# Performance work log

Measured on AMD Instinct MI355X. Metric: run time of the kernel, lower is better.

Reference implementation:

```python
import jax, jax.numpy as jnp
import numpy as np

NUM_HEADS = 8
TOPK = 16


def setup_inputs() -> dict:
    key = jax.random.key(0)
    ks = jax.random.split(key, 13)
    B, C, H, W = 2, 512, 64, 64
    Hu, Wu = H // 2, W // 2
    hd = C // NUM_HEADS
    n = lambda k, shape, s=1.0: jax.random.normal(k, shape, dtype=jnp.float32) * s
    return {
        "x": n(ks[0], (B, C, H, W)),
        "upper_feat": n(ks[1], (B, C, Hu, Wu)),
        "gumbel": jax.random.gumbel(ks[2], (B, NUM_HEADS, Hu * Wu), dtype=jnp.float32),
        # 1x1 convs (Conv2d + folded eval-mode BN => weight matrix + bias)
        "q_w": n(ks[3], (C, C), 0.02), "q_b": n(ks[4], (C,), 0.02),
        "kv_w": n(ks[5], (2 * C, C), 0.02), "kv_b": n(ks[6], (2 * C,), 0.02),
        "proj_w": n(ks[7], (C, C), 0.02), "proj_b": n(ks[8], (C,), 0.02),
        # depthwise 7x7 PE conv (groups = C)
        "pe_w": n(ks[9], (C, 1, 7, 7), 0.02), "pe_b": n(ks[10], (C,), 0.02),
        # gate conv1d kernel_size=1: [head_dim, 2*head_dim]
        "gate_w": n(ks[11], (hd, 2 * hd), 0.02), "gate_b": n(ks[12], (hd,), 0.02),
    }


def reference(x, upper_feat, gumbel, q_w, q_b, kv_w, kv_b, proj_w, proj_b,
              pe_w, pe_b, gate_w, gate_b):
    B, C, H, W = x.shape
    hd = C // NUM_HEADS
    Hu, Wu = upper_feat.shape[2], upper_feat.shape[3]
    N, Nu = H * W, Hu * Wu
    scale = hd ** -0.5

    def conv1x1(t, w, b):
        return jnp.einsum('bchw,oc->bohw', t, w) + b[None, :, None, None]

    # coarse attention: q from x, k/v from upper_feat
    q = conv1x1(x, q_w, q_b).reshape(B, NUM_HEADS, hd, N).transpose(0, 1, 3, 2)          # [B,h,N,d]
    kv = conv1x1(upper_feat, kv_w, kv_b).reshape(B, NUM_HEADS, 2 * hd, Nu).transpose(0, 1, 3, 2)
    k, v = kv[..., :hd], kv[..., hd:]                                                    # [B,h,Nu,d]
    sim = jnp.einsum('bhnd,bhmd->bhnm', q, k) * scale                                    # [B,h,N,Nu]
    attn = jax.nn.softmax(sim, axis=-1)
    coarse = jnp.einsum('bhnm,bhmd->bhnd', attn, v)                                      # [B,h,N,d]

    # fine branch: kv from x, top-k token selection via gumbel-softmax scores
    f_kv = conv1x1(x, kv_w, kv_b).reshape(B, NUM_HEADS, 2 * hd, N).transpose(0, 1, 3, 2)
    f_k, f_v = f_kv[..., :hd], f_kv[..., hd:]                                            # [B,h,N,d]

    # heat: channel-mean of x, adaptive-avg-pooled 2x2 to upper resolution (no grad)
    heat = jax.lax.stop_gradient(
        x.mean(axis=1).reshape(B, Hu, 2, Wu, 2).mean(axis=(2, 4)).reshape(B, Nu))
    global_sim = sim.mean(axis=2) * heat[:, None, :]                                     # [B,h,Nu]
    soft_weights = jax.nn.softmax(global_sim + gumbel, axis=-1)
    _, idx = jax.lax.top_k(soft_weights, TOPK)                                           # [B,h,K]

    # map each selected upper-token to its 2x2 block of x-tokens
    h_idx = (idx // Wu) * 2
    w_idx = (idx % Wu) * 2
    idx_full = jnp.concatenate(
        [(h_idx + dh) * W + (w_idx + dw) for dh in range(2) for dw in range(2)], axis=-1)  # [B,h,4K]

    topk_k = jnp.take_along_axis(f_k, idx_full[..., None], axis=2)                       # [B,h,4K,d]
    topk_v = jnp.take_along_axis(f_v, idx_full[..., None], axis=2)
    fine = jax.nn.softmax(jnp.einsum('bhnd,bhmd->bhnm', q, topk_k) * scale, axis=-1)
    refined = jnp.einsum('bhnm,bhmd->bhnd', fine, topk_v)                                # [B,h,N,d]

    # gated fusion (conv1d kernel_size=1 == per-token linear over 2d channels)
    fusion = jnp.concatenate([coarse, refined], axis=-1)                                 # [B,h,N,2d]
    gate = jax.nn.sigmoid(jnp.einsum('bhnc,oc->bhno', fusion, gate_w) + gate_b)
    out = gate * refined + (1.0 - gate) * coarse                                         # [B,h,N,d]

    x_out = out.transpose(0, 1, 3, 2).reshape(B, C, H, W)

    # positional encoding: depthwise 7x7 conv on v, bilinear upsample to (H,W)
    v_rs = v.transpose(0, 1, 3, 2).reshape(B, C, Hu, Wu)
    v_pe = jax.lax.conv_general_dilated(
        v_rs, pe_w, (1, 1), ((3, 3), (3, 3)), feature_group_count=C,
        dimension_numbers=('NCHW', 'OIHW', 'NCHW')) + pe_b[None, :, None, None]
    v_pe = jax.image.resize(v_pe, (B, C, H, W), method='bilinear')

    return conv1x1(x_out + v_pe, proj_w, proj_b)
```

## Files before the change

### kernel.cpp

```cpp
#include <hip/hip_runtime.h>
#include <hip/hip_bf16.h>
#include <cstdint>

typedef __hip_bfloat16 bf16;
typedef unsigned short u16;
typedef __attribute__((ext_vector_type(8))) short bf16x8;
typedef __attribute__((ext_vector_type(4))) float f32x4;

static __device__ __forceinline__ float bs2f(u16 s) {
  unsigned int u = ((unsigned int)s) << 16;
  float f;
  __builtin_memcpy(&f, &u, 4);
  return f;
}
static __device__ __forceinline__ u16 f2bs(float f) {
  bf16 h = __float2bfloat16(f);
  u16 s;
  __builtin_memcpy(&s, &h, 2);
  return s;
}
static __device__ __forceinline__ float ldf(const void* p, size_t i, int f32) {
  return f32 ? ((const float*)p)[i] : bs2f(((const u16*)p)[i]);
}

__global__ __launch_bounds__(256) void detect_dtype(const uint4* __restrict__ xs,
                                                    int* __restrict__ flag) {
  int i = blockIdx.x * 256 + threadIdx.x;
  uint4 v = xs[i];
  bool hit = false;
#pragma unroll
  for (int j = 0; j < 4; ++j) {
    unsigned w = (j == 0) ? v.x : (j == 1) ? v.y : (j == 2) ? v.z : v.w;
    if ((w & 0x7F80u) == 0x7F80u) hit = true;
    if ((w & 0x7F800000u) == 0x7F800000u) hit = true;
  }
  unsigned long long mask = __ballot(hit);
  if (mask != 0ull && (threadIdx.x & 63) == 0) atomicOr(flag, 1);
}

__global__ __launch_bounds__(256) void prep_gate(
    const void* __restrict__ gate_w, const void* __restrict__ gate_b,
    u16* __restrict__ gwb, float* __restrict__ gbf,
    const int* __restrict__ dtf) {
  const int f32 = *dtf;
  int t = threadIdx.x;
  for (int i = t; i < 8192; i += 256)
    gwb[i] = f32 ? f2bs(((const float*)gate_w)[i]) : ((const u16*)gate_w)[i];
  if (t < 64) gbf[t] = ldf(gate_b, t, f32);
}

__global__ __launch_bounds__(256) void transpose_bf16(
    const void* __restrict__ src, u16* __restrict__ dst, int N,
    float* __restrict__ heat, const int* __restrict__ dtf) {
  const int f32 = *dtf;
  const int b = blockIdx.z, n0 = blockIdx.x * 64, c0 = blockIdx.y * 64;
  const int t = threadIdx.x;
  __shared__ __align__(16) u16 tile[64][72];
#pragma unroll
  for (int j = 0; j < 2; ++j) {
    int cc = (t >> 3) + j * 32;
    int nn = (t & 7) * 8;
    u16 tmp[8];
    if (f32) {
      const float* s4 = (const float*)src + ((size_t)(b * 512 + c0 + cc)) * N + n0 + nn;
#pragma unroll
      for (int u = 0; u < 8; ++u) tmp[u] = f2bs(s4[u]);
    } else {
      *reinterpret_cast<uint4*>(tmp) = *reinterpret_cast<const uint4*>(
          (const u16*)src + ((size_t)(b * 512 + c0 + cc)) * N + n0 + nn);
    }
    *reinterpret_cast<uint4*>(&tile[cc][nn]) = *reinterpret_cast<const uint4*>(tmp);
  }
  __syncthreads();
  if (heat != nullptr && t < 32) {
    float s = 0.f;
#pragma unroll 8
    for (int cc = 0; cc < 64; ++cc)
      s += bs2f(tile[cc][2 * t]) + bs2f(tile[cc][2 * t + 1]);
    int y = blockIdx.x;
    atomicAdd(&heat[b * 1024 + (y >> 1) * 32 + t], s);
  }
#pragma unroll
  for (int j = 0; j < 2; ++j) {
    int nn = (t >> 3) + j * 32;
    int cc0 = (t & 7) * 8;
    u16 tmp[8];
#pragma unroll
    for (int u = 0; u < 8; ++u) tmp[u] = tile[cc0 + u][nn];
    *reinterpret_cast<uint4*>(&dst[((size_t)b * N + n0 + nn) * 512 + c0 + cc0]) =
        *reinterpret_cast<const uint4*>(tmp);
  }
}

template<int MODE>
__global__ __launch_bounds__(256) void gemm128(
    const u16* __restrict__ A, const void* __restrict__ W,
    const void* __restrict__ bias, u16* __restrict__ o0,
    void* __restrict__ ob, float* __restrict__ qsum, int M,
    const int* __restrict__ dtf) {
  const int f32 = *dtf;
  const int b = blockIdx.z, m0 = blockIdx.x * 128, oo0 = blockIdx.y * 64;
  const int t = threadIdx.x, w = t >> 6, lane = t & 63;
  const int quad = lane >> 4, c = lane & 15;
  __shared__ __align__(16) u16 As[128][72];
  __shared__ __align__(16) u16 Ws[64][72];
  f32x4 acc[2][4];
#pragma unroll
  for (int nt = 0; nt < 2; ++nt)
#pragma unroll
    for (int ot = 0; ot < 4; ++ot) acc[nt][ot] = (f32x4){0.f, 0.f, 0.f, 0.f};
  const u16* Ab = A + (size_t)b * M * 512;
  const int arow = t >> 1, acol = (t & 1) * 32;
  const int wrow = t >> 2, wcol = (t & 3) * 16;

  for (int k0 = 0; k0 < 512; k0 += 64) {
    __syncthreads();
    {
      const u16* ga = Ab + (size_t)(m0 + arow) * 512 + k0 + acol;
      uint4* ad = reinterpret_cast<uint4*>(&As[arow][acol]);
      const uint4* gs = reinterpret_cast<const uint4*>(ga);
      ad[0] = gs[0]; ad[1] = gs[1]; ad[2] = gs[2]; ad[3] = gs[3];
      if (f32) {
        const float* gw = (const float*)W + (size_t)(oo0 + wrow) * 512 + k0 + wcol;
#pragma unroll
        for (int e = 0; e < 16; ++e) Ws[wrow][wcol + e] = f2bs(gw[e]);
      } else {
        const u16* gw = (const u16*)W + (size_t)(oo0 + wrow) * 512 + k0 + wcol;
        *reinterpret_cast<uint4*>(&Ws[wrow][wcol])     = *reinterpret_cast<const uint4*>(gw);
        *reinterpret_cast<uint4*>(&Ws[wrow][wcol + 8]) = *reinterpret_cast<const uint4*>(gw + 8);
      }
    }
    __syncthreads();
#pragma unroll
    for (int ks = 0; ks < 2; ++ks) {
      bf16x8 av[2];
      av[0] = *reinterpret_cast<const bf16x8*>(&As[w * 32 + c][ks * 32 + quad * 8]);
      av[1] = *reinterpret_cast<const bf16x8*>(&As[w * 32 + 16 + c][ks * 32 + quad * 8]);
#pragma unroll
      for (int ot = 0; ot < 4; ++ot) {
        bf16x8 wv = *reinterpret_cast<const bf16x8*>(&Ws[ot * 16 + c][ks * 32 + quad * 8]);
#pragma unroll
        for (int nt = 0; nt < 2; ++nt) {
          if (MODE == 3)
            acc[nt][ot] = __builtin_amdgcn_mfma_f32_16x16x32_bf16(wv, av[nt], acc[nt][ot], 0, 0, 0);
          else
            acc[nt][ot] = __builtin_amdgcn_mfma_f32_16x16x32_bf16(av[nt], wv, acc[nt][ot], 0, 0, 0);
        }
      }
    }
  }

  if (MODE == 0) {
    const int h = oo0 >> 6, bh = b * 8 + h;
#pragma unroll
    for (int ot = 0; ot < 4; ++ot) {
      int o = oo0 + ot * 16 + c;
      int d = o & 63;
      float bv = ldf(bias, o, f32);
      float qs = 0.f;
#pragma unroll
      for (int nt = 0; nt < 2; ++nt)
#pragma unroll
        for (int r = 0; r < 4; ++r) {
          int m = m0 + w * 32 + nt * 16 + quad * 4 + r;
          u16 val = f2bs(acc[nt][ot][r] + bv);
          o0[((size_t)bh * M + m) * 64 + d] = val;
          qs += bs2f(val);
        }
      qs += __shfl_xor(qs, 16, 64);
      qs += __shfl_xor(qs, 32, 64);
      if (quad == 0) atomicAdd(&qsum[bh * 64 + d], qs);
    }
  } else {
#pragma unroll
    for (int ot = 0; ot < 4; ++ot)
#pragma unroll
      for (int r = 0; r < 4; ++r) {
        int o = oo0 + ot * 16 + quad * 4 + r;
        float bv = ldf(bias, o, f32);
#pragma unroll
        for (int nt = 0; nt < 2; ++nt) {
          int m = m0 + w * 32 + nt * 16 + c;
          float val = acc[nt][ot][r] + bv;
          size_t oi_ = ((size_t)(b * 512 + o)) * M + m;
          if (f32) ((float*)ob)[oi_] = val;
          else     ((u16*)ob)[oi_] = f2bs(val);
        }
      }
  }
}

__global__ __launch_bounds__(256) void gemm_kv(
    const u16* __restrict__ A, const void* __restrict__ W,
    const void* __restrict__ bias, u16* __restrict__ kb, u16* __restrict__ vTb,
    int M, const int* __restrict__ dtf) {
  const int f32 = *dtf;
  const int b = blockIdx.z, m0 = blockIdx.x * 64, oo0 = blockIdx.y * 64;
  const int t = threadIdx.x, w = t >> 6, lane = t & 63;
  const int quad = lane >> 4, c = lane & 15;
  __shared__ __align__(16) u16 As[64][72];
  __shared__ __align__(16) u16 Ws[64][72];
  f32x4 acc[4];
#pragma unroll
  for (int ot = 0; ot < 4; ++ot) acc[ot] = (f32x4){0.f, 0.f, 0.f, 0.f};
  const u16* Ab = A + (size_t)b * M * 512;
  const int srow = t >> 2, scol = (t & 3) * 16;

  for (int k0 = 0; k0 < 512; k0 += 64) {
    __syncthreads();
    {
      const u16* ga = Ab + (size_t)(m0 + srow) * 512 + k0 + scol;
      *reinterpret_cast<uint4*>(&As[srow][scol])     = *reinterpret_cast<const uint4*>(ga);
      *reinterpret_cast<uint4*>(&As[srow][scol + 8]) = *reinterpret_cast<const uint4*>(ga + 8);
      if (f32) {
        const float* gw = (const float*)W + (size_t)(oo0 + srow) * 512 + k0 + scol;
#pragma unroll
        for (int e = 0; e < 16; ++e) Ws[srow][scol + e] = f2bs(gw[e]);
      } else {
        const u16* gw = (const u16*)W + (size_t)(oo0 + srow) * 512 + k0 + scol;
        *reinterpret_cast<uint4*>(&Ws[srow][scol])     = *reinterpret_cast<const uint4*>(gw);
        *reinterpret_cast<uint4*>(&Ws[srow][scol + 8]) = *reinterpret_cast<const uint4*>(gw + 8);
      }
    }
    __syncthreads();
#pragma unroll
    for (int ks = 0; ks < 2; ++ks) {
      bf16x8 av = *reinterpret_cast<const bf16x8*>(&As[w * 16 + c][ks * 32 + quad * 8]);
#pragma unroll
      for (int ot = 0; ot < 4; ++ot) {
        bf16x8 wv = *reinterpret_cast<const bf16x8*>(&Ws[ot * 16 + c][ks * 32 + quad * 8]);
        acc[ot] = __builtin_amdgcn_mfma_f32_16x16x32_bf16(av, wv, acc[ot], 0, 0, 0);
      }
    }
  }

#pragma unroll
  for (int ot = 0; ot < 4; ++ot) {
    int o = oo0 + ot * 16 + c;
    float bv = ldf(bias, o, f32);
    int hh = o >> 7, jj = o & 127;
#pragma unroll
    for (int r = 0; r < 4; ++r) {
      int m = m0 + w * 16 + quad * 4 + r;
      u16 val = f2bs(acc[ot][r] + bv);
      if (jj < 64) kb[((size_t)(b * 8 + hh) * M + m) * 64 + jj] = val;
      else         vTb[((size_t)(b * 8 + hh) * 64 + (jj & 63)) * M + m] = val;
    }
  }
}

__global__ __launch_bounds__(256) void topk_kernel(
    const float* __restrict__ qsum, const u16* __restrict__ k,
    const float* __restrict__ heat, const void* __restrict__ gumbel,
    int* __restrict__ posb, const int* __restrict__ dtf) {
  const int f32 = *dtf;
  int bh = blockIdx.x, b = bh >> 3, t = threadIdx.x;
  __shared__ float qs[64];
  __shared__ float s[1024];
  __shared__ float rv[256];
  __shared__ int   ri[256];
  if (t < 64) qs[t] = qsum[bh * 64 + t];
  __syncthreads();
  for (int j = 0; j < 4; ++j) {
    int m = t + j * 256;
    const u16* kr = k + ((size_t)bh * 1024 + m) * 64;
    float dot = 0.f;
    for (int d = 0; d < 64; ++d) dot += qs[d] * bs2f(kr[d]);
    s[m] = dot * (0.125f / 4096.0f) * (heat[b * 1024 + m] * (1.0f / 2048.0f)) +
           ldf(gumbel, (size_t)bh * 1024 + m, f32);
  }
  __syncthreads();
  for (int it = 0; it < 16; ++it) {
    float bv = -1e30f; int bi = 0x7fffffff;
    for (int j = 0; j < 4; ++j) {
      int m = t + j * 256; float vv = s[m];
      if (vv > bv || (vv == bv && m < bi)) { bv = vv; bi = m; }
    }
    rv[t] = bv; ri[t] = bi; __syncthreads();
    for (int off = 128; off; off >>= 1) {
      if (t < off) {
        if (rv[t + off] > rv[t] || (rv[t + off] == rv[t] && ri[t + off] < ri[t])) {
          rv[t] = rv[t + off]; ri[t] = ri[t + off];
        }
      }
      __syncthreads();
    }
    if (t == 0) {
      int mi = ri[0]; s[mi] = -1e30f;
      int hy = (mi >> 5) * 2, wx = (mi & 31) * 2;
      posb[bh * 64 + it]      = hy * 64 + wx;
      posb[bh * 64 + 16 + it] = hy * 64 + wx + 1;
      posb[bh * 64 + 32 + it] = (hy + 1) * 64 + wx;
      posb[bh * 64 + 48 + it] = (hy + 1) * 64 + wx + 1;
    }
    __syncthreads();
  }
}

__global__ __launch_bounds__(256) void gather_kv_mfma(
    const u16* __restrict__ xT, const void* __restrict__ kv_w,
    const void* __restrict__ kv_b, const int* __restrict__ posb,
    u16* __restrict__ tkb, u16* __restrict__ tvTb,
    const int* __restrict__ dtf) {
  const int f32 = *dtf;
  const int bh = blockIdx.x, b = bh >> 3, h = bh & 7;
  const int half = blockIdx.y;
  const int t = threadIdx.x, w = t >> 6, lane = t & 63;
  const int quad = lane >> 4, c = lane & 15;
  __shared__ int pos[64];
  __shared__ __align__(16) u16 As[64][72];
  __shared__ __align__(16) u16 Ws[64][72];
  if (t < 64) pos[t] = posb[bh * 64 + t];
  __syncthreads();
  const int obase = h * 128 + half * 64;
  const int srow = t >> 2, scol = (t & 3) * 16;
  const int arow = pos[srow];
  f32x4 acc[4];
#pragma unroll
  for (int ot = 0; ot < 4; ++ot) acc[ot] = (f32x4){0.f, 0.f, 0.f, 0.f};

  for (int k0 = 0; k0 < 512; k0 += 64) {
    __syncthreads();
    {
      const u16* ga = xT + ((size_t)b * 4096 + arow) * 512 + k0 + scol;
      *reinterpret_cast<uint4*>(&As[srow][scol])     = *reinterpret_cast<const uint4*>(ga);
      *reinterpret_cast<uint4*>(&As[srow][scol + 8]) = *reinterpret_cast<const uint4*>(ga + 8);
      if (f32) {
        const float* gw = (const float*)kv_w + (size_t)(obase + srow) * 512 + k0 + scol;
#pragma unroll
        for (int e = 0; e < 16; ++e) Ws[srow][scol + e] = f2bs(gw[e]);
      } else {
        const u16* gw = (const u16*)kv_w + (size_t)(obase + srow) * 512 + k0 + scol;
        *reinterpret_cast<uint4*>(&Ws[srow][scol])     = *reinterpret_cast<const uint4*>(gw);
        *reinterpret_cast<uint4*>(&Ws[srow][scol + 8]) = *reinterpret_cast<const uint4*>(gw + 8);
      }
    }
    __syncthreads();
#pragma unroll
    for (int ks = 0; ks < 2; ++ks) {
      bf16x8 av = *reinterpret_cast<const bf16x8*>(&As[w * 16 + c][ks * 32 + quad * 8]);
#pragma unroll
      for (int ot = 0; ot < 4; ++ot) {
        bf16x8 wv = *reinterpret_cast<const bf16x8*>(&Ws[ot * 16 + c][ks * 32 + quad * 8]);
        acc[ot] = __builtin_amdgcn_mfma_f32_16x16x32_bf16(av, wv, acc[ot], 0, 0, 0);
      }
    }
  }

#pragma unroll
  for (int ot = 0; ot < 4; ++ot) {
    int d = ot * 16 + c;
    float bv = ldf(kv_b, obase + d, f32);
#pragma unroll
    for (int r = 0; r < 4; ++r) {
      int m = w * 16 + quad * 4 + r;
      u16 val = f2bs(acc[ot][r] + bv);
      if (half) tvTb[((size_t)bh * 64 + d) * 64 + m] = val;
      else      tkb[((size_t)bh * 64 + m) * 64 + d] = val;
    }
  }
}

__global__ __launch_bounds__(256) void coarse_attn_mfma(
    const u16* __restrict__ q, const u16* __restrict__ k,
    const u16* __restrict__ vT, u16* __restrict__ coarse) {
  const int bh = blockIdx.y;
  const int n0 = blockIdx.x * 128;
  const int t = threadIdx.x, w = t >> 6, lane = t & 63;
  const int quad = lane >> 4, c = lane & 15;
  __shared__ __align__(16) u16 Ks[2][64][72];
  __shared__ __align__(16) u16 Vt[2][64][72];
  __shared__ __align__(16) u16 Ps[4][2][16][72];

  bf16x8 bq[2][2];
#pragma unroll
  for (int nt = 0; nt < 2; ++nt) {
    const u16* qr = q + ((size_t)bh * 4096 + n0 + w * 32 + nt * 16 + c) * 64;
    bq[nt][0] = *reinterpret_cast<const bf16x8*>(qr + quad * 8);
    bq[nt][1] = *reinterpret_cast<const bf16x8*>(qr + 32 + quad * 8);
  }
  f32x4 po[2][4];
#pragma unroll
  for (int nt = 0; nt < 2; ++nt)
#pragma unroll
    for (int dt = 0; dt < 4; ++dt) po[nt][dt] = (f32x4){0.f, 0.f, 0.f, 0.f};
  float sume[2] = {0.f, 0.f};

  const u16* kbase = k + (size_t)bh * 65536;
  const u16* vbase = vT + (size_t)bh * 65536;
  const int srow = t >> 2, scol = (t & 3) * 16;

  uint4 kr0, kr1, vr0, vr1;
  {
    const u16* gk = kbase + (size_t)srow * 64 + scol;
    kr0 = *reinterpret_cast<const uint4*>(gk);
    kr1 = *reinterpret_cast<const uint4*>(gk + 8);
    const u16* gv = vbase + (size_t)srow * 1024 + scol;
    vr0 = *reinterpret_cast<const uint4*>(gv);
    vr1 = *reinterpret_cast<const uint4*>(gv + 8);
    *reinterpret_cast<uint4*>(&Ks[0][srow][scol])     = kr0;
    *reinterpret_cast<uint4*>(&Ks[0][srow][scol + 8]) = kr1;
    *reinterpret_cast<uint4*>(&Vt[0][srow][scol])     = vr0;
    *reinterpret_cast<uint4*>(&Vt[0][srow][scol + 8]) = vr1;
  }

  for (int ch = 0; ch < 16; ++ch) {
    __syncthreads();
    const int buf = ch & 1;
    if (ch + 1 < 16) {
      int m1 = (ch + 1) * 64;
      const u16* gk = kbase + (size_t)(m1 + srow) * 64 + scol;
      kr0 = *reinterpret_cast<const uint4*>(gk);
      kr1 = *reinterpret_cast<const uint4*>(gk + 8);
      const u16* gv = vbase + (size_t)srow * 1024 + m1 + scol;
      vr0 = *reinterpret_cast<const uint4*>(gv);
      vr1 = *reinterpret_cast<const uint4*>(gv + 8);
    }

    f32x4 st[2][4];
#pragma unroll
    for (int mt = 0; mt < 4; ++mt) {
      bf16x8 ak0 = *reinterpret_cast<const bf16x8*>(&Ks[buf][mt * 16 + c][quad * 8]);
      bf16x8 ak1 = *reinterpret_cast<const bf16x8*>(&Ks[buf][mt * 16 + c][32 + quad * 8]);
#pragma unroll
      for (int nt = 0; nt < 2; ++nt) {
        f32x4 acc = (f32x4){0.f, 0.f, 0.f, 0.f};
        acc = __builtin_amdgcn_mfma_f32_16x16x32_bf16(ak0, bq[nt][0], acc, 0, 0, 0);
        acc = __builtin_amdgcn_mfma_f32_16x16x32_bf16(ak1, bq[nt][1], acc, 0, 0, 0);
        st[nt][mt] = acc;
      }
    }
#pragma unroll
    for (int nt = 0; nt < 2; ++nt) {
      float cs = 0.f;
#pragma unroll
      for (int mt = 0; mt < 4; ++mt) {
        float e0 = __expf(st[nt][mt][0] * 0.125f);
        float e1 = __expf(st[nt][mt][1] * 0.125f);
        float e2 = __expf(st[nt][mt][2] * 0.125f);
        float e3 = __expf(st[nt][mt][3] * 0.125f);
        cs += (e0 + e1) + (e2 + e3);
        ushort4 pw;
        pw.x = f2bs(e0); pw.y = f2bs(e1); pw.z = f2bs(e2); pw.w = f2bs(e3);
        *reinterpret_cast<ushort4*>(&Ps[w][nt][c][mt * 16 + quad * 4]) = pw;
      }
      cs += __shfl_xor(cs, 16, 64);
      cs += __shfl_xor(cs, 32, 64);
      sume[nt] += cs;
    }
#pragma unroll
    for (int s = 0; s < 2; ++s) {
      bf16x8 bp0 = *reinterpret_cast<const bf16x8*>(&Ps[w][0][c][s * 32 + quad * 8]);
      bf16x8 bp1 = *reinterpret_cast<const bf16x8*>(&Ps[w][1][c][s * 32 + quad * 8]);
#pragma unroll
      for (int dt = 0; dt < 4; ++dt) {
        bf16x8 av = *reinterpret_cast<const bf16x8*>(&Vt[buf][dt * 16 + c][s * 32 + quad * 8]);
        po[0][dt] = __builtin_amdgcn_mfma_f32_16x16x32_bf16(av, bp0, po[0][dt], 0, 0, 0);
        po[1][dt] = __builtin_amdgcn_mfma_f32_16x16x32_bf16(av, bp1, po[1][dt], 0, 0, 0);
      }
    }

    if (ch + 1 < 16) {
      const int nb = buf ^ 1;
      *reinterpret_cast<uint4*>(&Ks[nb][srow][scol])     = kr0;
      *reinterpret_cast<uint4*>(&Ks[nb][srow][scol + 8]) = kr1;
      *reinterpret_cast<uint4*>(&Vt[nb][srow][scol])     = vr0;
      *reinterpret_cast<uint4*>(&Vt[nb][srow][scol + 8]) = vr1;
    }
  }

#pragma unroll
  for (int nt = 0; nt < 2; ++nt) {
    float inv = 1.0f / sume[nt];
    u16* orow = coarse + ((size_t)bh * 4096 + n0 + w * 32 + nt * 16 + c) * 64;
#pragma unroll
    for (int dt = 0; dt < 4; ++dt) {
      ushort4 r;
      r.x = f2bs(po[nt][dt][0] * inv); r.y = f2bs(po[nt][dt][1] * inv);
      r.z = f2bs(po[nt][dt][2] * inv); r.w = f2bs(po[nt][dt][3] * inv);
      *reinterpret_cast<ushort4*>(&orow[dt * 16 + quad * 4]) = r;
    }
  }
}

__global__ __launch_bounds__(256) void dwconv_kernel(
    const u16* __restrict__ vT, const void* __restrict__ pe_w,
    const void* __restrict__ pe_b, u16* __restrict__ vpe,
    const int* __restrict__ dtf) {
  const int f32 = *dtf;
  int bc = blockIdx.x;
  int b = bc >> 9, c = bc & 511;
  int h = c >> 6, d = c & 63;
  int t = threadIdx.x;
  __shared__ float img[1024];
  __shared__ float wts[49];
  const u16* base = vT + ((size_t)(b * 8 + h) * 64 + d) * 1024;
  if (t < 128) {
    uint4 v4 = reinterpret_cast<const uint4*>(base)[t];
    u16 tmp[8];
    *reinterpret_cast<uint4*>(tmp) = v4;
#pragma unroll
    for (int e = 0; e < 8; ++e) img[t * 8 + e] = bs2f(tmp[e]);
  }
  if (t < 49) wts[t] = ldf(pe_w, c * 49 + t, f32);
  float bias = ldf(pe_b, c, f32);
  __syncthreads();
  for (int i = t; i < 1024; i += 256) {
    int y = i >> 5, xx = i & 31;
    float a = 0.f;
#pragma unroll
    for (int ky = 0; ky < 7; ++ky) {
      int yy = y + ky - 3;
      if ((unsigned)yy >= 32u) continue;
#pragma unroll
      for (int kx = 0; kx < 7; ++kx) {
        int xc = xx + kx - 3;
        if ((unsigned)xc >= 32u) continue;
        a += img[yy * 32 + xc] * wts[ky * 7 + kx];
      }
    }
    vpe[(size_t)bc * 1024 + i] = f2bs(a + bias);
  }
}

__global__ __launch_bounds__(256) void fine_mfma(
    const u16* __restrict__ q, const u16* __restrict__ tkb,
    const u16* __restrict__ tvTb, const u16* __restrict__ co,
    const u16* __restrict__ gwb, const float* __restrict__ gbf,
    const u16* __restrict__ vpe, u16* __restrict__ xsT) {
  const int bh = blockIdx.y, b = bh >> 3, h = bh & 7;
  const int y = blockIdx.x;
  const int n0 = y * 64;
  const int t = threadIdx.x, w = t >> 6, lane = t & 63;
  const int quad = lane >> 4, c = lane & 15;

  __shared__ __align__(16) u16 fus[4][16][136];
  __shared__ __align__(16) u16 vl[2][64][40];
  __shared__ float gbl[64];

  int jy = y >> 1, y0, y1; float wy0, wy1;
  if ((y & 1) == 0) { y0 = (jy > 0) ? jy - 1 : 0; y1 = jy; wy0 = 0.25f; wy1 = 0.75f; }
  else              { y0 = jy; y1 = (jy < 31) ? jy + 1 : 31; wy0 = 0.75f; wy1 = 0.25f; }

  for (int idx = t; idx < 512; idx += 256) {
    int seg = idx & 3, ch = (idx >> 2) & 63, r = idx >> 8;
    int yy = r ? y1 : y0;
    const uint4* src = reinterpret_cast<const uint4*>(
        vpe + ((size_t)(b * 512 + h * 64 + ch)) * 1024 + yy * 32);
    *reinterpret_cast<uint4*>(&vl[r][ch][seg * 8]) = src[seg];
  }
  if (t < 64) gbl[t] = gbf[t];

  const int n = n0 + w * 16 + c;
  bf16x8 bq[2];
  {
    const u16* qr = q + ((size_t)bh * 4096 + n) * 64;
    bq[0] = *reinterpret_cast<const bf16x8*>(qr + quad * 8);
    bq[1] = *reinterpret_cast<const bf16x8*>(qr + 32 + quad * 8);
  }
  __syncthreads();

  f32x4 st[4];
#pragma unroll
  for (int mt = 0; mt < 4; ++mt) {
    f32x4 acc = (f32x4){0.f, 0.f, 0.f, 0.f};
#pragma unroll
    for (int s = 0; s < 2; ++s) {
      bf16x8 ak = *reinterpret_cast<const bf16x8*>(
          &tkb[((size_t)bh * 64 + mt * 16 + c) * 64 + s * 32 + quad * 8]);
      acc = __builtin_amdgcn_mfma_f32_16x16x32_bf16(ak, bq[s], acc, 0, 0, 0);
    }
    st[mt] = acc;
  }
  float sume = 0.f;
#pragma unroll
  for (int mt = 0; mt < 4; ++mt) {
    float e0 = __expf(st[mt][0] * 0.125f);
    float e1 = __expf(st[mt][1] * 0.125f);
    float e2 = __expf(st[mt][2] * 0.125f);
    float e3 = __expf(st[mt][3] * 0.125f);
    sume += (e0 + e1) + (e2 + e3);
    ushort4 pw;
    pw.x = f2bs(e0); pw.y = f2bs(e1); pw.z = f2bs(e2); pw.w = f2bs(e3);
    *reinterpret_cast<ushort4*>(&fus[w][c][mt * 16 + quad * 4]) = pw;
  }
  sume += __shfl_xor(sume, 16, 64);
  sume += __shfl_xor(sume, 32, 64);
  float inv = 1.0f / sume;

  f32x4 po[4];
#pragma unroll
  for (int dt = 0; dt < 4; ++dt) po[dt] = (f32x4){0.f, 0.f, 0.f, 0.f};
#pragma unroll
  for (int s = 0; s < 2; ++s) {
    bf16x8 bp = *reinterpret_cast<const bf16x8*>(&fus[w][c][s * 32 + quad * 8]);
#pragma unroll
    for (int dt = 0; dt < 4; ++dt) {
      bf16x8 av = *reinterpret_cast<const bf16x8*>(
          &tvTb[((size_t)bh * 64 + dt * 16 + c) * 64 + s * 32 + quad * 8]);
      po[dt] = __builtin_amdgcn_mfma_f32_16x16x32_bf16(av, bp, po[dt], 0, 0, 0);
    }
  }

  {
    const u16* crow = co + ((size_t)bh * 4096 + n) * 64 + quad * 16;
    *reinterpret_cast<uint4*>(&fus[w][c][quad * 16])     = *reinterpret_cast<const uint4*>(crow);
    *reinterpret_cast<uint4*>(&fus[w][c][quad * 16 + 8]) = *reinterpret_cast<const uint4*>(crow + 8);
  }
#pragma unroll
  for (int dt = 0; dt < 4; ++dt) {
    ushort4 rw;
    rw.x = f2bs(po[dt][0] * inv); rw.y = f2bs(po[dt][1] * inv);
    rw.z = f2bs(po[dt][2] * inv); rw.w = f2bs(po[dt][3] * inv);
    *reinterpret_cast<ushort4*>(&fus[w][c][64 + dt * 16 + quad * 4]) = rw;
  }

  f32x4 ga[4];
#pragma unroll
  for (int ot = 0; ot < 4; ++ot) ga[ot] = (f32x4){0.f, 0.f, 0.f, 0.f};
#pragma unroll
  for (int s = 0; s < 4; ++s) {
    bf16x8 bf = *reinterpret_cast<const bf16x8*>(&fus[w][c][s * 32 + quad * 8]);
#pragma unroll
    for (int ot = 0; ot < 4; ++ot) {
      bf16x8 ag = *reinterpret_cast<const bf16x8*>(
          gwb + (ot * 16 + c) * 128 + s * 32 + quad * 8);
      ga[ot] = __builtin_amdgcn_mfma_f32_16x16x32_bf16(ag, bf, ga[ot], 0, 0, 0);
    }
  }

  const int x = w * 16 + c;
  int jx = x >> 1, x0, x1; float wx0, wx1;
  if ((x & 1) == 0) { x0 = (jx > 0) ? jx - 1 : 0; x1 = jx; wx0 = 0.25f; wx1 = 0.75f; }
  else              { x0 = jx; x1 = (jx < 31) ? jx + 1 : 31; wx0 = 0.75f; wx1 = 0.25f; }
#pragma unroll
  for (int dt = 0; dt < 4; ++dt) {
    ushort4 ow;
    u16 tmp[4];
#pragma unroll
    for (int r = 0; r < 4; ++r) {
      int row = dt * 16 + quad * 4 + r;
      float ref = po[dt][r] * inv;
      float coar = bs2f(fus[w][c][row]);
      float g = 1.0f / (1.0f + __expf(-(ga[dt][r] + gbl[row])));
      float vv = wy0 * (wx0 * bs2f(vl[0][row][x0]) + wx1 * bs2f(vl[0][row][x1])) +
                 wy1 * (wx0 * bs2f(vl[1][row][x0]) + wx1 * bs2f(vl[1][row][x1]));
      tmp[r] = f2bs(g * ref + (1.0f - g) * coar + vv);
    }
    ow.x = tmp[0]; ow.y = tmp[1]; ow.z = tmp[2]; ow.w = tmp[3];
    *reinterpret_cast<ushort4*>(&fus[w][c][dt * 16 + quad * 4]) = ow;
  }

  {
    int nl = lane >> 2, cs = (lane & 3) * 16;
    u16* dst = xsT + ((size_t)b * 4096 + n0 + w * 16 + nl) * 512 + h * 64 + cs;
    *reinterpret_cast<uint4*>(dst)     = *reinterpret_cast<const uint4*>(&fus[w][nl][cs]);
    *reinterpret_cast<uint4*>(dst + 8) = *reinterpret_cast<const uint4*>(&fus[w][nl][cs + 8]);
  }
}

extern "C" void kernel_launch(void* const* d_in, const int* in_sizes, int n_in,
                              void* d_out, int out_size, void* d_ws, size_t ws_size,
                              hipStream_t stream) {
  const void* x    = d_in[0];
  const void* up   = d_in[1];
  const void* gum  = d_in[2];
  const void* q_w  = d_in[3];
  const void* q_b  = d_in[4];
  const void* kv_w = d_in[5];
  const void* kv_b = d_in[6];
  const void* p_w  = d_in[7];
  const void* p_b  = d_in[8];
  const void* pe_w = d_in[9];
  const void* pe_b = d_in[10];
  const void* g_w  = d_in[11];
  const void* g_b  = d_in[12];

  float* ws    = (float*)d_ws;
  int*   dtf   = (int*)ws;
  float* qsum  = ws + 16;
  float* heat  = qsum + 1024;
  int*   posb  = (int*)(heat + 2048);
  float* gbf   = (float*)(posb + 1024);
  u16*   gwb   = (u16*)(gbf + 64);
  u16*   tkb   = gwb + 8192;
  u16*   tvTb  = tkb + 65536;
  u16*   qb    = tvTb + 65536;
  u16*   kb    = qb + 4194304;
  u16*   vTb   = kb + 1048576;
  u16*   xT    = vTb + 1048576;
  u16*   upT   = xT + 4194304;
  u16*   co    = upT + 1048576;
  u16*   xsT   = co + 4194304;
  u16*   vpe   = xsT + 4194304;

  dim3 blk(256);
  hipMemsetAsync(ws, 0, (16 + 1024 + 2048) * 4, stream);
  detect_dtype<<<dim3(64), blk, 0, stream>>>((const uint4*)x, dtf);
  prep_gate<<<dim3(1), blk, 0, stream>>>(g_w, g_b, gwb, gbf, dtf);
  transpose_bf16<<<dim3(64, 8, 2), blk, 0, stream>>>(x, xT, 4096, heat, dtf);
  transpose_bf16<<<dim3(16, 8, 2), blk, 0, stream>>>(up, upT, 1024, nullptr, dtf);
  gemm128<0><<<dim3(32, 8, 2), blk, 0, stream>>>(xT, q_w, q_b, qb, nullptr, qsum, 4096, dtf);
  gemm_kv<<<dim3(16, 16, 2), blk, 0, stream>>>(upT, kv_w, kv_b, kb, vTb, 1024, dtf);
  topk_kernel<<<dim3(16), blk, 0, stream>>>(qsum, kb, heat, gum, posb, dtf);
  gather_kv_mfma<<<dim3(16, 2), blk, 0, stream>>>(xT, kv_w, kv_b, posb, tkb, tvTb, dtf);
  coarse_attn_mfma<<<dim3(32, 16), blk, 0, stream>>>(qb, kb, vTb, co);
  dwconv_kernel<<<dim3(1024), blk, 0, stream>>>(vTb, pe_w, pe_b, vpe, dtf);
  fine_mfma<<<dim3(64, 16), blk, 0, stream>>>(qb, tkb, tvTb, co, gwb, gbf, vpe, xsT);
  gemm128<3><<<dim3(32, 8, 2), blk, 0, stream>>>(xsT, p_w, p_b, nullptr, d_out, nullptr, 4096, dtf);
}
```

Measured before the change: 271.7 us.

## Fuse coarse attention with fine attention and gated fusion kernel

Merges the coarse attention kernel into the fine-attention/gating kernel, so coarse outputs stay in registers instead of being written to and re-read from a global buffer. Each block now covers 128 tokens (two image rows), reuses one LDS arena for K/V staging and then fusion scratch, and loads three rows of the upsampled PE source. This removes one launch and about 8 MB of intermediate traffic. In exchange the fused kernel holds more live registers and has a longer serial tail per block, with fewer blocks for the fine phase.

```diff
diff --git a/kernel.cpp b/kernel.cpp
--- a/kernel.cpp
+++ b/kernel.cpp
@@ -361,128 +361,6 @@
   }
 }
 
-__global__ __launch_bounds__(256) void coarse_attn_mfma(
-    const u16* __restrict__ q, const u16* __restrict__ k,
-    const u16* __restrict__ vT, u16* __restrict__ coarse) {
-  const int bh = blockIdx.y;
-  const int n0 = blockIdx.x * 128;
-  const int t = threadIdx.x, w = t >> 6, lane = t & 63;
-  const int quad = lane >> 4, c = lane & 15;
-  __shared__ __align__(16) u16 Ks[2][64][72];
-  __shared__ __align__(16) u16 Vt[2][64][72];
-  __shared__ __align__(16) u16 Ps[4][2][16][72];
-
-  bf16x8 bq[2][2];
-#pragma unroll
-  for (int nt = 0; nt < 2; ++nt) {
-    const u16* qr = q + ((size_t)bh * 4096 + n0 + w * 32 + nt * 16 + c) * 64;
-    bq[nt][0] = *reinterpret_cast<const bf16x8*>(qr + quad * 8);
-    bq[nt][1] = *reinterpret_cast<const bf16x8*>(qr + 32 + quad * 8);
-  }
-  f32x4 po[2][4];
-#pragma unroll
-  for (int nt = 0; nt < 2; ++nt)
-#pragma unroll
-    for (int dt = 0; dt < 4; ++dt) po[nt][dt] = (f32x4){0.f, 0.f, 0.f, 0.f};
-  float sume[2] = {0.f, 0.f};
-
-  const u16* kbase = k + (size_t)bh * 65536;
-  const u16* vbase = vT + (size_t)bh * 65536;
-  const int srow = t >> 2, scol = (t & 3) * 16;
-
-  uint4 kr0, kr1, vr0, vr1;
-  {
-    const u16* gk = kbase + (size_t)srow * 64 + scol;
-    kr0 = *reinterpret_cast<const uint4*>(gk);
-    kr1 = *reinterpret_cast<const uint4*>(gk + 8);
-    const u16* gv = vbase + (size_t)srow * 1024 + scol;
-    vr0 = *reinterpret_cast<const uint4*>(gv);
-    vr1 = *reinterpret_cast<const uint4*>(gv + 8);
-    *reinterpret_cast<uint4*>(&Ks[0][srow][scol])     = kr0;
-    *reinterpret_cast<uint4*>(&Ks[0][srow][scol + 8]) = kr1;
-    *reinterpret_cast<uint4*>(&Vt[0][srow][scol])     = vr0;
-    *reinterpret_cast<uint4*>(&Vt[0][srow][scol + 8]) = vr1;
-  }
-
-  for (int ch = 0; ch < 16; ++ch) {
-    __syncthreads();
-    const int buf = ch & 1;
-    if (ch + 1 < 16) {
-      int m1 = (ch + 1) * 64;
-      const u16* gk = kbase + (size_t)(m1 + srow) * 64 + scol;
-      kr0 = *reinterpret_cast<const uint4*>(gk);
-      kr1 = *reinterpret_cast<const uint4*>(gk + 8);
-      const u16* gv = vbase + (size_t)srow * 1024 + m1 + scol;
-      vr0 = *reinterpret_cast<const uint4*>(gv);
-      vr1 = *reinterpret_cast<const uint4*>(gv + 8);
-    }
-
-    f32x4 st[2][4];
-#pragma unroll
-    for (int mt = 0; mt < 4; ++mt) {
-      bf16x8 ak0 = *reinterpret_cast<const bf16x8*>(&Ks[buf][mt * 16 + c][quad * 8]);
-      bf16x8 ak1 = *reinterpret_cast<const bf16x8*>(&Ks[buf][mt * 16 + c][32 + quad * 8]);
-#pragma unroll
-      for (int nt = 0; nt < 2; ++nt) {
-        f32x4 acc = (f32x4){0.f, 0.f, 0.f, 0.f};
-        acc = __builtin_amdgcn_mfma_f32_16x16x32_bf16(ak0, bq[nt][0], acc, 0, 0, 0);
-        acc = __builtin_amdgcn_mfma_f32_16x16x32_bf16(ak1, bq[nt][1], acc, 0, 0, 0);
-        st[nt][mt] = acc;
-      }
-    }
-#pragma unroll
-    for (int nt = 0; nt < 2; ++nt) {
-      float cs = 0.f;
-#pragma unroll
-      for (int mt = 0; mt < 4; ++mt) {
-        float e0 = __expf(st[nt][mt][0] * 0.125f);
-        float e1 = __expf(st[nt][mt][1] * 0.125f);
-        float e2 = __expf(st[nt][mt][2] * 0.125f);
-        float e3 = __expf(st[nt][mt][3] * 0.125f);
-        cs += (e0 + e1) + (e2 + e3);
-        ushort4 pw;
-        pw.x = f2bs(e0); pw.y = f2bs(e1); pw.z = f2bs(e2); pw.w = f2bs(e3);
-        *reinterpret_cast<ushort4*>(&Ps[w][nt][c][mt * 16 + quad * 4]) = pw;
-      }
-      cs += __shfl_xor(cs, 16, 64);
-      cs += __shfl_xor(cs, 32, 64);
-      sume[nt] += cs;
-    }
-#pragma unroll
-    for (int s = 0; s < 2; ++s) {
-      bf16x8 bp0 = *reinterpret_cast<const bf16x8*>(&Ps[w][0][c][s * 32 + quad * 8]);
-      bf16x8 bp1 = *reinterpret_cast<const bf16x8*>(&Ps[w][1][c][s * 32 + quad * 8]);
-#pragma unroll
-      for (int dt = 0; dt < 4; ++dt) {
-        bf16x8 av = *reinterpret_cast<const bf16x8*>(&Vt[buf][dt * 16 + c][s * 32 + quad * 8]);
-        po[0][dt] = __builtin_amdgcn_mfma_f32_16x16x32_bf16(av, bp0, po[0][dt], 0, 0, 0);
-        po[1][dt] = __builtin_amdgcn_mfma_f32_16x16x32_bf16(av, bp1, po[1][dt], 0, 0, 0);
-      }
-    }
-
-    if (ch + 1 < 16) {
-      const int nb = buf ^ 1;
-      *reinterpret_cast<uint4*>(&Ks[nb][srow][scol])     = kr0;
-      *reinterpret_cast<uint4*>(&Ks[nb][srow][scol + 8]) = kr1;
-      *reinterpret_cast<uint4*>(&Vt[nb][srow][scol])     = vr0;
-      *reinterpret_cast<uint4*>(&Vt[nb][srow][scol + 8]) = vr1;
-    }
-  }
-
-#pragma unroll
-  for (int nt = 0; nt < 2; ++nt) {
-    float inv = 1.0f / sume[nt];
-    u16* orow = coarse + ((size_t)bh * 4096 + n0 + w * 32 + nt * 16 + c) * 64;
-#pragma unroll
-    for (int dt = 0; dt < 4; ++dt) {
-      ushort4 r;
-      r.x = f2bs(po[nt][dt][0] * inv); r.y = f2bs(po[nt][dt][1] * inv);
-      r.z = f2bs(po[nt][dt][2] * inv); r.w = f2bs(po[nt][dt][3] * inv);
-      *reinterpret_cast<ushort4*>(&orow[dt * 16 + quad * 4]) = r;
-    }
-  }
-}
-
 __global__ __launch_bounds__(256) void dwconv_kernel(
     const u16* __restrict__ vT, const void* __restrict__ pe_w,
     const void* __restrict__ pe_b, u16* __restrict__ vpe,
@@ -523,139 +401,243 @@
   }
 }
 
-__global__ __launch_bounds__(256) void fine_mfma(
-    const u16* __restrict__ q, const u16* __restrict__ tkb,
-    const u16* __restrict__ tvTb, const u16* __restrict__ co,
-    const u16* __restrict__ gwb, const float* __restrict__ gbf,
-    const u16* __restrict__ vpe, u16* __restrict__ xsT) {
+__global__ __launch_bounds__(256) void attn_fused(
+    const u16* __restrict__ q, const u16* __restrict__ k,
+    const u16* __restrict__ vT, const u16* __restrict__ tkb,
+    const u16* __restrict__ tvTb, const u16* __restrict__ gwb,
+    const float* __restrict__ gbf, const u16* __restrict__ vpe,
+    u16* __restrict__ xsT) {
   const int bh = blockIdx.y, b = bh >> 3, h = bh & 7;
-  const int y = blockIdx.x;
-  const int n0 = y * 64;
+  const int bx = blockIdx.x;
+  const int n0 = bx * 128;
   const int t = threadIdx.x, w = t >> 6, lane = t & 63;
   const int quad = lane >> 4, c = lane & 15;
 
-  __shared__ __align__(16) u16 fus[4][16][136];
-  __shared__ __align__(16) u16 vl[2][64][40];
-  __shared__ float gbl[64];
-
-  int jy = y >> 1, y0, y1; float wy0, wy1;
-  if ((y & 1) == 0) { y0 = (jy > 0) ? jy - 1 : 0; y1 = jy; wy0 = 0.25f; wy1 = 0.75f; }
-  else              { y0 = jy; y1 = (jy < 31) ? jy + 1 : 31; wy0 = 0.75f; wy1 = 0.25f; }
-
-  for (int idx = t; idx < 512; idx += 256) {
-    int seg = idx & 3, ch = (idx >> 2) & 63, r = idx >> 8;
-    int yy = r ? y1 : y0;
+  __shared__ __align__(16) u16 lds[27648];
+  u16* Ks = lds;
+  u16* Vt = lds + 9216;
+  u16* Ps = lds + 18432;
+
+  bf16x8 bq[2][2];
+#pragma unroll
+  for (int nt = 0; nt < 2; ++nt) {
+    const u16* qr = q + ((size_t)bh * 4096 + n0 + w * 32 + nt * 16 + c) * 64;
+    bq[nt][0] = *reinterpret_cast<const bf16x8*>(qr + quad * 8);
+    bq[nt][1] = *reinterpret_cast<const bf16x8*>(qr + 32 + quad * 8);
+  }
+  f32x4 po[2][4];
+#pragma unroll
+  for (int nt = 0; nt < 2; ++nt)
+#pragma unroll
+    for (int dt = 0; dt < 4; ++dt) po[nt][dt] = (f32x4){0.f, 0.f, 0.f, 0.f};
+  float sume[2] = {0.f, 0.f};
+
+  const u16* kbase = k + (size_t)bh * 65536;
+  const u16* vbase = vT + (size_t)bh * 65536;
+  const int srow = t >> 2, scol = (t & 3) * 16;
+
+  uint4 kr0, kr1, vr0, vr1;
+  {
+    const u16* gk = kbase + (size_t)srow * 64 + scol;
+    kr0 = *reinterpret_cast<const uint4*>(gk);
+    kr1 = *reinterpret_cast<const uint4*>(gk + 8);
+    const u16* gv = vbase + (size_t)srow * 1024 + scol;
+    vr0 = *reinterpret_cast<const uint4*>(gv);
+    vr1 = *reinterpret_cast<const uint4*>(gv + 8);
+    *reinterpret_cast<uint4*>(&Ks[srow * 72 + scol])     = kr0;
+    *reinterpret_cast<uint4*>(&Ks[srow * 72 + scol + 8]) = kr1;
+    *reinterpret_cast<uint4*>(&Vt[srow * 72 + scol])     = vr0;
+    *reinterpret_cast<uint4*>(&Vt[srow * 72 + scol + 8]) = vr1;
+  }
+
+  for (int ch = 0; ch < 16; ++ch) {
+    __syncthreads();
+    const int buf = ch & 1;
+    if (ch + 1 < 16) {
+      int m1 = (ch + 1) * 64;
+      const u16* gk = kbase + (size_t)(m1 + srow) * 64 + scol;
+      kr0 = *reinterpret_cast<const uint4*>(gk);
+      kr1 = *reinterpret_cast<const uint4*>(gk + 8);
+      const u16* gv = vbase + (size_t)srow * 1024 + m1 + scol;
+      vr0 = *reinterpret_cast<const uint4*>(gv);
+      vr1 = *reinterpret_cast<const uint4*>(gv + 8);
+    }
+
+    f32x4 st[2][4];
+#pragma unroll
+    for (int mt = 0; mt < 4; ++mt) {
+      const u16* krow = &Ks[(buf * 64 + mt * 16 + c) * 72];
+      bf16x8 ak0 = *reinterpret_cast<const bf16x8*>(krow + quad * 8);
+      bf16x8 ak1 = *reinterpret_cast<const bf16x8*>(krow + 32 + quad * 8);
+#pragma unroll
+      for (int nt = 0; nt < 2; ++nt) {
+        f32x4 acc = (f32x4){0.f, 0.f, 0.f, 0.f};
+        acc = __builtin_amdgcn_mfma_f32_16x16x32_bf16(ak0, bq[nt][0], acc, 0, 0, 0);
+        acc = __builtin_amdgcn_mfma_f32_16x16x32_bf16(ak1, bq[nt][1], acc, 0, 0, 0);
+        st[nt][mt] = acc;
+      }
+    }
+#pragma unroll
+    for (int nt = 0; nt < 2; ++nt) {
+      float cs = 0.f;
+      u16* psw = &Ps[((w * 2 + nt) * 16 + c) * 72];
+#pragma unroll
+      for (int mt = 0; mt < 4; ++mt) {
+        float e0 = __expf(st[nt][mt][0] * 0.125f);
+        float e1 = __expf(st[nt][mt][1] * 0.125f);
+        float e2 = __expf(st[nt][mt][2] * 0.125f);
+        float e3 = __expf(st[nt][mt][3] * 0.125f);
+        cs += (e0 + e1) + (e2 + e3);
+        ushort4 pw;
+        pw.x = f2bs(e0); pw.y = f2bs(e1); pw.z = f2bs(e2); pw.w = f2bs(e3);
+        *reinterpret_cast<ushort4*>(psw + mt * 16 + quad * 4) = pw;
+      }
+      cs += __shfl_xor(cs, 16, 64);
+      cs += __shfl_xor(cs, 32, 64);
+      sume[nt] += cs;
+    }
+#pragma unroll
+    for (int s = 0; s < 2; ++s) {
+      bf16x8 bp0 = *reinterpret_cast<const bf16x8*>(&Ps[((w * 2 + 0) * 16 + c) * 72 + s * 32 + quad * 8]);
+      bf16x8 bp1 = *reinterpret_cast<const bf16x8*>(&Ps[((w * 2 + 1) * 16 + c) * 72 + s * 32 + quad * 8]);
+#pragma unroll
+      for (int dt = 0; dt < 4; ++dt) {
+        bf16x8 av = *reinterpret_cast<const bf16x8*>(&Vt[(buf * 64 + dt * 16 + c) * 72 + s * 32 + quad * 8]);
+        po[0][dt] = __builtin_amdgcn_mfma_f32_16x16x32_bf16(av, bp0, po[0][dt], 0, 0, 0);
+        po[1][dt] = __builtin_amdgcn_mfma_f32_16x16x32_bf16(av, bp1, po[1][dt], 0, 0, 0);
+      }
+    }
+
+    if (ch + 1 < 16) {
+      const int nb = buf ^ 1;
+      *reinterpret_cast<uint4*>(&Ks[(nb * 64 + srow) * 72 + scol])     = kr0;
+      *reinterpret_cast<uint4*>(&Ks[(nb * 64 + srow) * 72 + scol + 8]) = kr1;
+      *reinterpret_cast<uint4*>(&Vt[(nb * 64 + srow) * 72 + scol])     = vr0;
+      *reinterpret_cast<uint4*>(&Vt[(nb * 64 + srow) * 72 + scol + 8]) = vr1;
+    }
+  }
+
+  __syncthreads();
+  u16* fus = lds;
+  u16* vl  = lds + 17408;
+  float* gbl = (float*)(lds + 25088);
+
+  for (int idx = t; idx < 768; idx += 256) {
+    int seg = idx & 3, ch2 = (idx >> 2) & 63, r = idx >> 8;
+    int vrow = bx - 1 + r;
+    vrow = vrow < 0 ? 0 : (vrow > 31 ? 31 : vrow);
     const uint4* src = reinterpret_cast<const uint4*>(
-        vpe + ((size_t)(b * 512 + h * 64 + ch)) * 1024 + yy * 32);
-    *reinterpret_cast<uint4*>(&vl[r][ch][seg * 8]) = src[seg];
+        vpe + ((size_t)(b * 512 + h * 64 + ch2)) * 1024 + vrow * 32);
+    *reinterpret_cast<uint4*>(&vl[(r * 64 + ch2) * 40 + seg * 8]) = src[seg];
   }
   if (t < 64) gbl[t] = gbf[t];
-
-  const int n = n0 + w * 16 + c;
-  bf16x8 bq[2];
-  {
-    const u16* qr = q + ((size_t)bh * 4096 + n) * 64;
-    bq[0] = *reinterpret_cast<const bf16x8*>(qr + quad * 8);
-    bq[1] = *reinterpret_cast<const bf16x8*>(qr + 32 + quad * 8);
-  }
   __syncthreads();
 
-  f32x4 st[4];
-#pragma unroll
-  for (int mt = 0; mt < 4; ++mt) {
-    f32x4 acc = (f32x4){0.f, 0.f, 0.f, 0.f};
+  for (int nt = 0; nt < 2; ++nt) {
+    u16* fusw = &fus[((w * 2 + nt) * 16 + c) * 136];
+    f32x4 st[4];
+#pragma unroll
+    for (int mt = 0; mt < 4; ++mt) {
+      f32x4 acc = (f32x4){0.f, 0.f, 0.f, 0.f};
+#pragma unroll
+      for (int s = 0; s < 2; ++s) {
+        bf16x8 ak = *reinterpret_cast<const bf16x8*>(
+            &tkb[((size_t)bh * 64 + mt * 16 + c) * 64 + s * 32 + quad * 8]);
+        acc = __builtin_amdgcn_mfma_f32_16x16x32_bf16(ak, bq[nt][s], acc, 0, 0, 0);
+      }
+      st[mt] = acc;
+    }
+    float sume2 = 0.f;
+#pragma unroll
+    for (int mt = 0; mt < 4; ++mt) {
+      float e0 = __expf(st[mt][0] * 0.125f);
+      float e1 = __expf(st[mt][1] * 0.125f);
+      float e2 = __expf(st[mt][2] * 0.125f);
+      float e3 = __expf(st[mt][3] * 0.125f);
+      sume2 += (e0 + e1) + (e2 + e3);
+      ushort4 pw;
+      pw.x = f2bs(e0); pw.y = f2bs(e1); pw.z = f2bs(e2); pw.w = f2bs(e3);
+      *reinterpret_cast<ushort4*>(fusw + mt * 16 + quad * 4) = pw;
+    }
+    sume2 += __shfl_xor(sume2, 16, 64);
+    sume2 += __shfl_xor(sume2, 32, 64);
+    float inv2 = 1.0f / sume2;
+
+    f32x4 po2[4];
+#pragma unroll
+    for (int dt = 0; dt < 4; ++dt) po2[dt] = (f32x4){0.f, 0.f, 0.f, 0.f};
 #pragma unroll
     for (int s = 0; s < 2; ++s) {
-      bf16x8 ak = *reinterpret_cast<const bf16x8*>(
-          &tkb[((size_t)bh * 64 + mt * 16 + c) * 64 + s * 32 + quad * 8]);
-      acc = __builtin_amdgcn_mfma_f32_16x16x32_bf16(ak, bq[s], acc, 0, 0, 0);
-    }
-    st[mt] = acc;
-  }
-  float sume = 0.f;
-#pragma unroll
-  for (int mt = 0; mt < 4; ++mt) {
-    float e0 = __expf(st[mt][0] * 0.125f);
-    float e1 = __expf(st[mt][1] * 0.125f);
-    float e2 = __expf(st[mt][2] * 0.125f);
-    float e3 = __expf(st[mt][3] * 0.125f);
-    sume += (e0 + e1) + (e2 + e3);
-    ushort4 pw;
-    pw.x = f2bs(e0); pw.y = f2bs(e1); pw.z = f2bs(e2); pw.w = f2bs(e3);
-    *reinterpret_cast<ushort4*>(&fus[w][c][mt * 16 + quad * 4]) = pw;
-  }
-  sume += __shfl_xor(sume, 16, 64);
-  sume += __shfl_xor(sume, 32, 64);
-  float inv = 1.0f / sume;
-
-  f32x4 po[4];
-#pragma unroll
-  for (int dt = 0; dt < 4; ++dt) po[dt] = (f32x4){0.f, 0.f, 0.f, 0.f};
-#pragma unroll
-  for (int s = 0; s < 2; ++s) {
-    bf16x8 bp = *reinterpret_cast<const bf16x8*>(&fus[w][c][s * 32 + quad * 8]);
+      bf16x8 bp = *reinterpret_cast<const bf16x8*>(fusw + s * 32 + quad * 8);
+#pragma unroll
+      for (int dt = 0; dt < 4; ++dt) {
+        bf16x8 av = *reinterpret_cast<const bf16x8*>(
+            &tvTb[((size_t)bh * 64 + dt * 16 + c) * 64 + s * 32 + quad * 8]);
+        po2[dt] = __builtin_amdgcn_mfma_f32_16x16x32_bf16(av, bp, po2[dt], 0, 0, 0);
+      }
+    }
+
+    float invc = 1.0f / sume[nt];
 #pragma unroll
     for (int dt = 0; dt < 4; ++dt) {
-      bf16x8 av = *reinterpret_cast<const bf16x8*>(
-          &tvTb[((size_t)bh * 64 + dt * 16 + c) * 64 + s * 32 + quad * 8]);
-      po[dt] = __builtin_amdgcn_mfma_f32_16x16x32_bf16(av, bp, po[dt], 0, 0, 0);
-    }
-  }
-
-  {
-    const u16* crow = co + ((size_t)bh * 4096 + n) * 64 + quad * 16;
-    *reinterpret_cast<uint4*>(&fus[w][c][quad * 16])     = *reinterpret_cast<const uint4*>(crow);
-    *reinterpret_cast<uint4*>(&fus[w][c][quad * 16 + 8]) = *reinterpret_cast<const uint4*>(crow + 8);
-  }
-#pragma unroll
-  for (int dt = 0; dt < 4; ++dt) {
-    ushort4 rw;
-    rw.x = f2bs(po[dt][0] * inv); rw.y = f2bs(po[dt][1] * inv);
-    rw.z = f2bs(po[dt][2] * inv); rw.w = f2bs(po[dt][3] * inv);
-    *reinterpret_cast<ushort4*>(&fus[w][c][64 + dt * 16 + quad * 4]) = rw;
-  }
-
-  f32x4 ga[4];
-#pragma unroll
-  for (int ot = 0; ot < 4; ++ot) ga[ot] = (f32x4){0.f, 0.f, 0.f, 0.f};
-#pragma unroll
-  for (int s = 0; s < 4; ++s) {
-    bf16x8 bf = *reinterpret_cast<const bf16x8*>(&fus[w][c][s * 32 + quad * 8]);
-#pragma unroll
-    for (int ot = 0; ot < 4; ++ot) {
-      bf16x8 ag = *reinterpret_cast<const bf16x8*>(
-          gwb + (ot * 16 + c) * 128 + s * 32 + quad * 8);
-      ga[ot] = __builtin_amdgcn_mfma_f32_16x16x32_bf16(ag, bf, ga[ot], 0, 0, 0);
-    }
-  }
-
-  const int x = w * 16 + c;
-  int jx = x >> 1, x0, x1; float wx0, wx1;
-  if ((x & 1) == 0) { x0 = (jx > 0) ? jx - 1 : 0; x1 = jx; wx0 = 0.25f; wx1 = 0.75f; }
-  else              { x0 = jx; x1 = (jx < 31) ? jx + 1 : 31; wx0 = 0.75f; wx1 = 0.25f; }
-#pragma unroll
-  for (int dt = 0; dt < 4; ++dt) {
-    ushort4 ow;
-    u16 tmp[4];
-#pragma unroll
-    for (int r = 0; r < 4; ++r) {
-      int row = dt * 16 + quad * 4 + r;
-      float ref = po[dt][r] * inv;
-      float coar = bs2f(fus[w][c][row]);
-      float g = 1.0f / (1.0f + __expf(-(ga[dt][r] + gbl[row])));
-      float vv = wy0 * (wx0 * bs2f(vl[0][row][x0]) + wx1 * bs2f(vl[0][row][x1])) +
-                 wy1 * (wx0 * bs2f(vl[1][row][x0]) + wx1 * bs2f(vl[1][row][x1]));
-      tmp[r] = f2bs(g * ref + (1.0f - g) * coar + vv);
-    }
-    ow.x = tmp[0]; ow.y = tmp[1]; ow.z = tmp[2]; ow.w = tmp[3];
-    *reinterpret_cast<ushort4*>(&fus[w][c][dt * 16 + quad * 4]) = ow;
-  }
-
-  {
-    int nl = lane >> 2, cs = (lane & 3) * 16;
-    u16* dst = xsT + ((size_t)b * 4096 + n0 + w * 16 + nl) * 512 + h * 64 + cs;
-    *reinterpret_cast<uint4*>(dst)     = *reinterpret_cast<const uint4*>(&fus[w][nl][cs]);
-    *reinterpret_cast<uint4*>(dst + 8) = *reinterpret_cast<const uint4*>(&fus[w][nl][cs + 8]);
+      ushort4 cw, rw;
+      cw.x = f2bs(po[nt][dt][0] * invc); cw.y = f2bs(po[nt][dt][1] * invc);
+      cw.z = f2bs(po[nt][dt][2] * invc); cw.w = f2bs(po[nt][dt][3] * invc);
+      rw.x = f2bs(po2[dt][0] * inv2);    rw.y = f2bs(po2[dt][1] * inv2);
+      rw.z = f2bs(po2[dt][2] * inv2);    rw.w = f2bs(po2[dt][3] * inv2);
+      *reinterpret_cast<ushort4*>(fusw + dt * 16 + quad * 4)      = cw;
+      *reinterpret_cast<ushort4*>(fusw + 64 + dt * 16 + quad * 4) = rw;
+    }
+
+    f32x4 ga[4];
+#pragma unroll
+    for (int ot = 0; ot < 4; ++ot) ga[ot] = (f32x4){0.f, 0.f, 0.f, 0.f};
+#pragma unroll
+    for (int s = 0; s < 4; ++s) {
+      bf16x8 bf = *reinterpret_cast<const bf16x8*>(fusw + s * 32 + quad * 8);
+#pragma unroll
+      for (int ot = 0; ot < 4; ++ot) {
+        bf16x8 ag = *reinterpret_cast<const bf16x8*>(
+            gwb + (ot * 16 + c) * 128 + s * 32 + quad * 8);
+        ga[ot] = __builtin_amdgcn_mfma_f32_16x16x32_bf16(ag, bf, ga[ot], 0, 0, 0);
+      }
+    }
+
+    const int ylocal = (w * 32 + nt * 16) >> 6;
+    const int x = (w * 32 + nt * 16 + c) & 63;
+    float wy0, wy1; int i0, i1;
+    if (ylocal == 0) { wy0 = 0.25f; wy1 = 0.75f; i0 = (bx > 0) ? 0 : 1; i1 = 1; }
+    else             { wy0 = 0.75f; wy1 = 0.25f; i0 = 1; i1 = (bx < 31) ? 2 : 1; }
+    int jx = x >> 1, x0, x1; float wx0, wx1;
+    if ((x & 1) == 0) { x0 = (jx > 0) ? jx - 1 : 0; x1 = jx; wx0 = 0.25f; wx1 = 0.75f; }
+    else              { x0 = jx; x1 = (jx < 31) ? jx + 1 : 31; wx0 = 0.75f; wx1 = 0.25f; }
+#pragma unroll
+    for (int dt = 0; dt < 4; ++dt) {
+      ushort4 ow;
+      u16 tmp[4];
+#pragma unroll
+      for (int r = 0; r < 4; ++r) {
+        int row = dt * 16 + quad * 4 + r;
+        float ref = po2[dt][r] * inv2;
+        float coar = bs2f(fusw[row]);
+        float g = 1.0f / (1.0f + __expf(-(ga[dt][r] + gbl[row])));
+        float vv = wy0 * (wx0 * bs2f(vl[(i0 * 64 + row) * 40 + x0]) +
+                          wx1 * bs2f(vl[(i0 * 64 + row) * 40 + x1])) +
+                   wy1 * (wx0 * bs2f(vl[(i1 * 64 + row) * 40 + x0]) +
+                          wx1 * bs2f(vl[(i1 * 64 + row) * 40 + x1]));
+        tmp[r] = f2bs(g * ref + (1.0f - g) * coar + vv);
+      }
+      ow.x = tmp[0]; ow.y = tmp[1]; ow.z = tmp[2]; ow.w = tmp[3];
+      *reinterpret_cast<ushort4*>(fusw + dt * 16 + quad * 4) = ow;
+    }
+
+    {
+      int nl = lane >> 2, cs = (lane & 3) * 16;
+      const u16* srcrow = &fus[((w * 2 + nt) * 16 + nl) * 136 + cs];
+      u16* dst = xsT + ((size_t)b * 4096 + n0 + w * 32 + nt * 16 + nl) * 512 + h * 64 + cs;
+      *reinterpret_cast<uint4*>(dst)     = *reinterpret_cast<const uint4*>(srcrow);
+      *reinterpret_cast<uint4*>(dst + 8) = *reinterpret_cast<const uint4*>(srcrow + 8);
+    }
   }
 }
 
@@ -690,8 +672,7 @@
   u16*   vTb   = kb + 1048576;
   u16*   xT    = vTb + 1048576;
   u16*   upT   = xT + 4194304;
-  u16*   co    = upT + 1048576;
-  u16*   xsT   = co + 4194304;
+  u16*   xsT   = upT + 1048576;
   u16*   vpe   = xsT + 4194304;
 
   dim3 blk(256);
@@ -704,8 +685,7 @@
   gemm_kv<<<dim3(16, 16, 2), blk, 0, stream>>>(upT, kv_w, kv_b, kb, vTb, 1024, dtf);
   topk_kernel<<<dim3(16), blk, 0, stream>>>(qsum, kb, heat, gum, posb, dtf);
   gather_kv_mfma<<<dim3(16, 2), blk, 0, stream>>>(xT, kv_w, kv_b, posb, tkb, tvTb, dtf);
-  coarse_attn_mfma<<<dim3(32, 16), blk, 0, stream>>>(qb, kb, vTb, co);
   dwconv_kernel<<<dim3(1024), blk, 0, stream>>>(vTb, pe_w, pe_b, vpe, dtf);
-  fine_mfma<<<dim3(64, 16), blk, 0, stream>>>(qb, tkb, tvTb, co, gwb, gbf, vpe, xsT);
+  attn_fused<<<dim3(32, 16), blk, 0, stream>>>(qb, kb, vTb, tkb, tvTb, gwb, gbf, vpe, xsT);
   gemm128<3><<<dim3(32, 8, 2), blk, 0, stream>>>(xsT, p_w, p_b, nullptr, d_out, nullptr, 4096, dtf);
 }
```

Measured after the change: 263.9 us. -2.9%, faster.
